# Performance work log

Measured on AMD Instinct MI355X. Metric: run time of the kernel, lower is better.

## Reference

```python
import jax, jax.numpy as jnp
import numpy as np

EPS = 1e-4

def _ema(unit_embeddings, unit_confidence, unit_mask):
    # unit_embeddings: (B, J, D), unit_confidence/unit_mask: (B, J)
    emb_j = jnp.swapaxes(unit_embeddings, 0, 1)        # (J, B, D)
    p_j = jnp.swapaxes(unit_confidence, 0, 1)          # (J, B)
    m_j = jnp.swapaxes(unit_mask, 0, 1)                # (J, B)

    B, _, D = unit_embeddings.shape
    prev0 = jnp.zeros((B, D), dtype=unit_embeddings.dtype)

    def step(prev, inp):
        emb, p, m = inp                                # (B,D), (B,), (B,)
        p = jnp.clip(p, EPS, 1.0 - EPS)[:, None]       # (B,1)
        m = m[:, None]                                 # (B,1)
        cur = jnp.where(m, emb, jnp.zeros_like(emb))
        new = jnp.where(m, p * cur + (1.0 - p) * prev, prev)
        return new, new

    _, smoothed = jax.lax.scan(step, prev0, (emb_j, p_j, m_j))  # (J, B, D)
    return jnp.swapaxes(smoothed, 0, 1)                # (B, J, D)

def _upsample(smoothed, boundary_mask):
    # smoothed: (B, J, D), boundary_mask: (B, L) bool
    J = smoothed.shape[1]
    idx = jnp.cumsum(boundary_mask.astype(jnp.int32), axis=1) - 1
    idx = jnp.clip(idx, 0, J - 1)                      # (B, L)
    return jnp.take_along_axis(smoothed, idx[:, :, None], axis=1)  # (B, L, D)

def setup_inputs() -> dict:
    key = jax.random.key(0)
    k1, k2, k3, k4 = jax.random.split(key, 4)
    B, J, L, D = 16, 1024, 4096, 512
    unit_embeddings = jax.random.normal(k1, (B, J, D), dtype=jnp.float32)
    unit_confidence = jax.random.uniform(k2, (B, J), dtype=jnp.float32)
    unit_mask = jax.random.randint(k3, (B, J), 0, 2).astype(bool)
    boundary_mask = jax.random.randint(k4, (B, L), 0, 2).astype(bool)
    return {
        "unit_embeddings": unit_embeddings,
        "unit_confidence": unit_confidence,
        "unit_mask": unit_mask,
        "boundary_mask": boundary_mask,
    }

def reference(unit_embeddings, unit_confidence, unit_mask, boundary_mask):
    smoothed = _ema(unit_embeddings, unit_confidence, unit_mask)
    frames = _upsample(smoothed, boundary_mask)
    return frames
```

## Files before the change

### kernel.cpp

```cpp
#include <hip/hip_runtime.h>
#include <cstddef>

namespace {
constexpr int Bn = 16;
constexpr int Jn = 1024;
constexpr int Ln = 4096;
constexpr int Dn = 512;
constexpr int G  = 32;
constexpr int C  = Jn / G;
constexpr float kEps = 1e-4f;
}

__global__ void k_idx(const int* __restrict__ bnd, int* __restrict__ idx) {
  int b = blockIdx.x;
  int t = threadIdx.x;
  const int per = Ln / 256;
  const int* row = bnd + (size_t)b * Ln;
  int s = 0;
#pragma unroll
  for (int i = 0; i < per; ++i) s += (row[t * per + i] != 0) ? 1 : 0;

  __shared__ int sh[256];
  sh[t] = s;
  __syncthreads();
  for (int off = 1; off < 256; off <<= 1) {
    int v = (t >= off) ? sh[t - off] : 0;
    __syncthreads();
    sh[t] += v;
    __syncthreads();
  }
  int run = sh[t] - s;
#pragma unroll
  for (int i = 0; i < per; ++i) {
    run += (row[t * per + i] != 0) ? 1 : 0;
    int v = run - 1;
    v = v < 0 ? 0 : (v > Jn - 1 ? Jn - 1 : v);
    idx[(size_t)b * Ln + t * per + i] = v;
  }
}

__global__ void k_pass1(const float* __restrict__ emb, const float* __restrict__ conf,
                        const int* __restrict__ mask, float* __restrict__ local,
                        float* __restrict__ E, float* __restrict__ PA,
                        float* __restrict__ Ap) {
  int bc = blockIdx.x;
  int b = bc / C, c = bc % C;
  int d4 = threadIdx.x;
  int base = b * Jn + c * G;
  float4 s = make_float4(0.f, 0.f, 0.f, 0.f);
  float prod = 1.0f;
  for (int i = 0; i < G; ++i) {
    int j = base + i;
    float p = conf[j];
    p = fminf(fmaxf(p, kEps), 1.0f - kEps);
    bool m = (mask[j] != 0);
    float q = 1.0f - p;
    float4 e = ((const float4*)(emb + (size_t)j * Dn))[d4];
    if (m) {
      s.x = p * e.x + q * s.x;
      s.y = p * e.y + q * s.y;
      s.z = p * e.z + q * s.z;
      s.w = p * e.w + q * s.w;
      prod *= q;
    }
    ((float4*)(local + (size_t)j * Dn))[d4] = s;
    if (d4 == 0) PA[j] = prod;
  }
  ((float4*)(E + (size_t)bc * Dn))[d4] = s;
  if (d4 == 0) Ap[bc] = prod;
}

__global__ void k_chunk_start(const float* __restrict__ E, const float* __restrict__ Ap,
                              float* __restrict__ S) {
  int t = blockIdx.x * blockDim.x + threadIdx.x;
  if (t >= Bn * (Dn / 4)) return;
  int b = t / (Dn / 4), d4 = t % (Dn / 4);
  float4 s = make_float4(0.f, 0.f, 0.f, 0.f);
  for (int c = 0; c < C; ++c) {
    ((float4*)(S + ((size_t)(b * C + c)) * Dn))[d4] = s;
    float a = Ap[b * C + c];
    float4 e = ((const float4*)(E + ((size_t)(b * C + c)) * Dn))[d4];
    s.x = e.x + a * s.x;
    s.y = e.y + a * s.y;
    s.z = e.z + a * s.z;
    s.w = e.w + a * s.w;
  }
}

__global__ void k_gather(const float* __restrict__ local, const float* __restrict__ PA,
                         const float* __restrict__ S, const int* __restrict__ idx,
                         float* __restrict__ out) {
  size_t tid = (size_t)blockIdx.x * blockDim.x + threadIdx.x;
  int d4 = (int)(tid & (Dn / 4 - 1));
  size_t bl = tid >> 7;
  int j = idx[bl];
  size_t b = bl >> 12;
  int c = j >> 5;
  float pa = PA[b * Jn + (size_t)j];
  float4 sc = ((const float4*)(S + (b * C + (size_t)c) * Dn))[d4];
  float4 lo = ((const float4*)(local + (b * Jn + (size_t)j) * Dn))[d4];
  float4 o;
  o.x = lo.x + pa * sc.x;
  o.y = lo.y + pa * sc.y;
  o.z = lo.z + pa * sc.z;
  o.w = lo.w + pa * sc.w;
  ((float4*)out)[tid] = o;
}

extern "C" void kernel_launch(void* const* d_in, const int* in_sizes, int n_in,
                              void* d_out, int out_size, void* d_ws, size_t ws_size,
                              hipStream_t stream) {
  const float* emb  = (const float*)d_in[0];
  const float* conf = (const float*)d_in[1];
  const int*   mask = (const int*)d_in[2];
  const int*   bnd  = (const int*)d_in[3];
  float* out = (float*)d_out;

  float* ws = (float*)d_ws;
  float* local = ws;
  float* E   = local + (size_t)Bn * Jn * Dn;
  float* S   = E + (size_t)Bn * C * Dn;
  float* PA  = S + (size_t)Bn * C * Dn;
  float* Ap  = PA + (size_t)Bn * Jn;
  int*   idx = (int*)(Ap + Bn * C);

  hipLaunchKernelGGL(k_idx, dim3(Bn), dim3(256), 0, stream, bnd, idx);
  hipLaunchKernelGGL(k_pass1, dim3(Bn * C), dim3(Dn / 4), 0, stream,
                     emb, conf, mask, local, E, PA, Ap);
  hipLaunchKernelGGL(k_chunk_start, dim3((Bn * (Dn / 4) + 255) / 256), dim3(256), 0, stream,
                     E, Ap, S);
  size_t total4 = (size_t)Bn * Ln * (Dn / 4);
  hipLaunchKernelGGL(k_gather, dim3((unsigned)(total4 / 256)), dim3(256), 0, stream,
                     local, PA, S, idx, out);
}
```

Baseline: 187.6 us.

## Fuse index scan into pass1 kernel, shrink chunk-start blocks, swizzle gather blocks

Merges the boundary-index prefix-scan kernel into the chunked EMA pass1 kernel by adding extra blocks, which removes one launch and lets both run concurrently. The scan now uses 128 threads per row instead of 256. k_chunk_start now uses 64-thread blocks so its 2048 threads spread over more CUs, and it gets unrolling hints. k_gather remaps block IDs with an XCD-style swizzle so that neighbouring output rows land on the same die for cache locality. The risks are a longer serial scan per thread in the idx blocks and possible cache-locality changes from the swizzle.

```diff
diff --git a/kernel.cpp b/kernel.cpp
--- a/kernel.cpp
+++ b/kernel.cpp
@@ -9,73 +9,76 @@
 constexpr int G  = 32;
 constexpr int C  = Jn / G;
 constexpr float kEps = 1e-4f;
+constexpr int PASS1_BLOCKS = Bn * C;
 }
 
-__global__ void k_idx(const int* __restrict__ bnd, int* __restrict__ idx) {
-  int b = blockIdx.x;
+__global__ __launch_bounds__(128) void k_fused1(
+    const float* __restrict__ emb, const float* __restrict__ conf,
+    const int* __restrict__ mask, const int* __restrict__ bnd,
+    float* __restrict__ local, float* __restrict__ E,
+    float* __restrict__ PA, float* __restrict__ Ap, int* __restrict__ idx) {
+  int blk = blockIdx.x;
   int t = threadIdx.x;
-  const int per = Ln / 256;
-  const int* row = bnd + (size_t)b * Ln;
-  int s = 0;
-#pragma unroll
-  for (int i = 0; i < per; ++i) s += (row[t * per + i] != 0) ? 1 : 0;
+  if (blk < PASS1_BLOCKS) {
+    int b = blk / C, c = blk % C;
+    int base = b * Jn + c * G;
+    float4 s = make_float4(0.f, 0.f, 0.f, 0.f);
+    float prod = 1.0f;
+#pragma unroll 8
+    for (int i = 0; i < G; ++i) {
+      int j = base + i;
+      float p = conf[j];
+      p = fminf(fmaxf(p, kEps), 1.0f - kEps);
+      bool m = (mask[j] != 0);
+      float q = 1.0f - p;
+      float4 e = ((const float4*)(emb + (size_t)j * Dn))[t];
+      if (m) {
+        s.x = p * e.x + q * s.x;
+        s.y = p * e.y + q * s.y;
+        s.z = p * e.z + q * s.z;
+        s.w = p * e.w + q * s.w;
+        prod *= q;
+      }
+      ((float4*)(local + (size_t)j * Dn))[t] = s;
+      if (t == 0) PA[j] = prod;
+    }
+    ((float4*)(E + (size_t)blk * Dn))[t] = s;
+    if (t == 0) Ap[blk] = prod;
+  } else {
+    int b = blk - PASS1_BLOCKS;
+    const int per = Ln / 128;
+    const int* row = bnd + (size_t)b * Ln;
+    int s = 0;
+#pragma unroll 8
+    for (int i = 0; i < per; ++i) s += (row[t * per + i] != 0) ? 1 : 0;
 
-  __shared__ int sh[256];
-  sh[t] = s;
-  __syncthreads();
-  for (int off = 1; off < 256; off <<= 1) {
-    int v = (t >= off) ? sh[t - off] : 0;
+    __shared__ int sh[128];
+    sh[t] = s;
     __syncthreads();
-    sh[t] += v;
-    __syncthreads();
-  }
-  int run = sh[t] - s;
-#pragma unroll
-  for (int i = 0; i < per; ++i) {
-    run += (row[t * per + i] != 0) ? 1 : 0;
-    int v = run - 1;
-    v = v < 0 ? 0 : (v > Jn - 1 ? Jn - 1 : v);
-    idx[(size_t)b * Ln + t * per + i] = v;
+    for (int off = 1; off < 128; off <<= 1) {
+      int v = (t >= off) ? sh[t - off] : 0;
+      __syncthreads();
+      sh[t] += v;
+      __syncthreads();
+    }
+    int run = sh[t] - s;
+#pragma unroll 8
+    for (int i = 0; i < per; ++i) {
+      run += (row[t * per + i] != 0) ? 1 : 0;
+      int v = run - 1;
+      v = v < 0 ? 0 : (v > Jn - 1 ? Jn - 1 : v);
+      idx[(size_t)b * Ln + t * per + i] = v;
+    }
   }
 }
 
-__global__ void k_pass1(const float* __restrict__ emb, const float* __restrict__ conf,
-                        const int* __restrict__ mask, float* __restrict__ local,
-                        float* __restrict__ E, float* __restrict__ PA,
-                        float* __restrict__ Ap) {
-  int bc = blockIdx.x;
-  int b = bc / C, c = bc % C;
-  int d4 = threadIdx.x;
-  int base = b * Jn + c * G;
+__global__ __launch_bounds__(64) void k_chunk_start(
+    const float* __restrict__ E, const float* __restrict__ Ap,
+    float* __restrict__ S) {
+  int tg = blockIdx.x * 64 + threadIdx.x;
+  int b = tg / (Dn / 4), d4 = tg % (Dn / 4);
   float4 s = make_float4(0.f, 0.f, 0.f, 0.f);
-  float prod = 1.0f;
-  for (int i = 0; i < G; ++i) {
-    int j = base + i;
-    float p = conf[j];
-    p = fminf(fmaxf(p, kEps), 1.0f - kEps);
-    bool m = (mask[j] != 0);
-    float q = 1.0f - p;
-    float4 e = ((const float4*)(emb + (size_t)j * Dn))[d4];
-    if (m) {
-      s.x = p * e.x + q * s.x;
-      s.y = p * e.y + q * s.y;
-      s.z = p * e.z + q * s.z;
-      s.w = p * e.w + q * s.w;
-      prod *= q;
-    }
-    ((float4*)(local + (size_t)j * Dn))[d4] = s;
-    if (d4 == 0) PA[j] = prod;
-  }
-  ((float4*)(E + (size_t)bc * Dn))[d4] = s;
-  if (d4 == 0) Ap[bc] = prod;
-}
-
-__global__ void k_chunk_start(const float* __restrict__ E, const float* __restrict__ Ap,
-                              float* __restrict__ S) {
-  int t = blockIdx.x * blockDim.x + threadIdx.x;
-  if (t >= Bn * (Dn / 4)) return;
-  int b = t / (Dn / 4), d4 = t % (Dn / 4);
-  float4 s = make_float4(0.f, 0.f, 0.f, 0.f);
+#pragma unroll 8
   for (int c = 0; c < C; ++c) {
     ((float4*)(S + ((size_t)(b * C + c)) * Dn))[d4] = s;
     float a = Ap[b * C + c];
@@ -87,10 +90,13 @@
   }
 }
 
-__global__ void k_gather(const float* __restrict__ local, const float* __restrict__ PA,
-                         const float* __restrict__ S, const int* __restrict__ idx,
-                         float* __restrict__ out) {
-  size_t tid = (size_t)blockIdx.x * blockDim.x + threadIdx.x;
+__global__ __launch_bounds__(256) void k_gather(
+    const float* __restrict__ local, const float* __restrict__ PA,
+    const float* __restrict__ S, const int* __restrict__ idx,
+    float* __restrict__ out) {
+  unsigned bid = blockIdx.x;
+  unsigned sb = (bid & 7u) * 4096u + (bid >> 3);
+  size_t tid = (size_t)sb * 256 + threadIdx.x;
   int d4 = (int)(tid & (Dn / 4 - 1));
   size_t bl = tid >> 7;
   int j = idx[bl];
@@ -124,10 +130,9 @@
   float* Ap  = PA + (size_t)Bn * Jn;
   int*   idx = (int*)(Ap + Bn * C);
 
-  hipLaunchKernelGGL(k_idx, dim3(Bn), dim3(256), 0, stream, bnd, idx);
-  hipLaunchKernelGGL(k_pass1, dim3(Bn * C), dim3(Dn / 4), 0, stream,
-                     emb, conf, mask, local, E, PA, Ap);
-  hipLaunchKernelGGL(k_chunk_start, dim3((Bn * (Dn / 4) + 255) / 256), dim3(256), 0, stream,
+  hipLaunchKernelGGL(k_fused1, dim3(PASS1_BLOCKS + Bn), dim3(128), 0, stream,
+                     emb, conf, mask, bnd, local, E, PA, Ap, idx);
+  hipLaunchKernelGGL(k_chunk_start, dim3(Bn * (Dn / 4) / 64), dim3(64), 0, stream,
                      E, Ap, S);
   size_t total4 = (size_t)Bn * Ln * (Dn / 4);
   hipLaunchKernelGGL(k_gather, dim3((unsigned)(total4 / 256)), dim3(256), 0, stream,
```

Result: faster. 180.4 us (-3.9%).
